# Kernel tuning notes

Hardware: AMD Instinct MI355X
Metric: run time of the kernel (lower is better)

Reference implementation:

```python
import jax, jax.numpy as jnp
import numpy as np

B, L, H, S, EXP = 8, 2048, 256, 64, 2
E = H * EXP

def setup_inputs() -> dict:
    key = jax.random.key(0)
    ks = jax.random.split(key, 12)
    u = jax.random.normal(ks[0], (B, L, H), dtype=jnp.float32)
    W_in = jax.random.normal(ks[1], (H, 2 * E), dtype=jnp.float32) * 0.02
    b_in = jax.random.normal(ks[2], (2 * E,), dtype=jnp.float32) * 0.02
    conv_w = jax.random.normal(ks[3], (E, 3), dtype=jnp.float32) * 0.3  # depthwise k=3
    conv_b = jax.random.normal(ks[4], (E,), dtype=jnp.float32) * 0.02
    W_x = jax.random.normal(ks[5], (E, 3 * S), dtype=jnp.float32) * 0.02
    b_x = jax.random.normal(ks[6], (3 * S,), dtype=jnp.float32) * 0.02
    A_log = jax.random.normal(ks[7], (S,), dtype=jnp.float32) * 0.1
    Dp = jnp.ones((E,), dtype=jnp.float32)
    W_out = jax.random.normal(ks[8], (E, H), dtype=jnp.float32) * 0.02
    b_out = jax.random.normal(ks[9], (H,), dtype=jnp.float32) * 0.02
    ln_g = jnp.ones((E,), dtype=jnp.float32)
    ln_b = jnp.zeros((E,), dtype=jnp.float32)
    return {"u": u, "W_in": W_in, "b_in": b_in, "conv_w": conv_w, "conv_b": conv_b,
            "W_x": W_x, "b_x": b_x, "A_log": A_log, "Dp": Dp,
            "W_out": W_out, "b_out": b_out, "ln_g": ln_g, "ln_b": ln_b}

def reference(u, W_in, b_in, conv_w, conv_b, W_x, b_x, A_log, Dp, W_out, b_out, ln_g, ln_b):
    Bb, Ll, Hh = u.shape
    Ss = A_log.shape[0]
    Ee = Dp.shape[0]
    xz = u @ W_in + b_in                      # [B,L,2E]
    x, z = jnp.split(xz, 2, axis=-1)          # [B,L,E] each
    # depthwise conv1d, kernel=3, padding=1 along L
    xp = jnp.pad(x, ((0, 0), (1, 1), (0, 0)))
    x = xp[:, :-2] * conv_w[:, 0] + xp[:, 1:-1] * conv_w[:, 1] + xp[:, 2:] * conv_w[:, 2] + conv_b
    x = jax.nn.silu(x)
    ssm = x @ W_x + b_x                       # [B,L,3S]
    delta, Bm, Cm = jnp.split(ssm, 3, axis=-1)
    delta = jax.nn.softplus(delta)            # [B,L,S]
    A = -jnp.exp(jnp.clip(A_log, -5.0, 5.0))  # [S]
    # torch broadcast quirk: delta[...,None] * A[None,None,:] -> [B,L,S,S], entry = delta[b,l,i]*A[j]
    A_d = jnp.exp(jnp.clip(delta[:, :, :, None] * A[None, None, None, :], -10.0, 0.0))  # [B,L,S,S]
    # bmm(B_discrete, x[:,t,:,None]) == (delta*B) * sum_e x, broadcast over E
    inp_term = (delta * Bm) * x.sum(-1, keepdims=True)  # [B,L,S]

    def step(h, inputs):
        A_t, it_t, C_t, x_t = inputs          # [B,S,S],[B,S],[B,S],[B,E]
        h = jnp.einsum('bij,bje->bie', A_t, h) + it_t[:, :, None]
        h = jnp.clip(h, -100.0, 100.0)
        y = jnp.einsum('bse,bs->be', h, C_t) + Dp * x_t
        return h, y

    h0 = jnp.zeros((Bb, Ss, Ee), dtype=u.dtype)
    xs = (jnp.swapaxes(A_d, 0, 1), jnp.swapaxes(inp_term, 0, 1),
          jnp.swapaxes(Cm, 0, 1), jnp.swapaxes(x, 0, 1))
    _, ys = jax.lax.scan(step, h0, xs)
    outputs = jnp.swapaxes(ys, 0, 1)          # [B,L,E]
    mu = outputs.mean(-1, keepdims=True)
    var = ((outputs - mu) ** 2).mean(-1, keepdims=True)
    y = (outputs - mu) / jnp.sqrt(var + 1e-5) * ln_g + ln_b
    y = y * jax.nn.silu(z)
    return y @ W_out + b_out  # dropout is identity in eval mode
```

## Files before the change

kernel.cpp:

```cpp
#include <hip/hip_runtime.h>
#include <hip/hip_bf16.h>

constexpr int BB = 8;
constexpr int LLEN = 2048;
constexpr int HH = 256;
constexpr int EE = 512;
constexpr int MM = BB * LLEN;

typedef short bf16x8 __attribute__((ext_vector_type(8)));
typedef float f32x4  __attribute__((ext_vector_type(4)));

static __device__ inline unsigned short f2bf(float f) {
    unsigned u = __builtin_bit_cast(unsigned, f);
    unsigned r = (u + 0x7FFFu + ((u >> 16) & 1u)) >> 16;
    return (unsigned short)r;
}
static __device__ inline float bf2f(unsigned short h) {
    return __builtin_bit_cast(float, (unsigned)h << 16);
}

#define GL2LDS(gp, lp) __builtin_amdgcn_global_load_lds( \
    (const __attribute__((address_space(1))) void*)(gp), \
    (__attribute__((address_space(3))) void*)(lp), 16, 0, 0)

__global__ __launch_bounds__(256) void cast_bf16_kernel(
    const float* __restrict__ in, unsigned short* __restrict__ out)
{
    int b = blockIdx.x;
    int cpx = gridDim.x >> 3;
    int lin = (b & 7) * cpx + (b >> 3);
    int i = (lin * 256 + threadIdx.x) * 4;
    float4 v = *reinterpret_cast<const float4*>(in + i);
    ushort4 o = {f2bf(v.x), f2bf(v.y), f2bf(v.z), f2bf(v.w)};
    *reinterpret_cast<ushort4*>(out + i) = o;
}

__global__ __launch_bounds__(256) void transpose_cast_kernel(
    const float* __restrict__ W, unsigned short* __restrict__ Wt, int K, int N)
{
    int i = blockIdx.x * 256 + threadIdx.x;
    if (i < K * N) {
        int n = i / K, k = i - n * K;
        Wt[i] = f2bf(W[(size_t)k * N + n]);
    }
}

__global__ __launch_bounds__(256) void k1_gemm(
    const unsigned short* __restrict__ A, const unsigned short* __restrict__ Bt,
    const float* __restrict__ bias,
    unsigned short* __restrict__ xb, unsigned short* __restrict__ zsb)
{
    __shared__ unsigned short Al[128 * 32];
    __shared__ unsigned short Bl[128 * 32];

    const int tid = threadIdx.x;
    const int lane = tid & 63;
    const int wave = tid >> 6;
    const int wrow = wave >> 1, wcol = wave & 1;
    const int l15 = lane & 15;
    const int lk  = lane >> 4;

    const int cpx = gridDim.x >> 3;
    int lin = blockIdx.x;
    lin = (lin & 7) * cpx + (lin >> 3);
    const int row0 = (lin >> 3) * 128;
    const int col0 = (lin & 7) * 128;
    const bool zside = col0 >= EE;
    unsigned short* Cp = zside ? zsb : xb;
    const int cb = zside ? col0 - EE : col0;

    f32x4 acc[4][4] = {};

    #pragma unroll
    for (int t = 0; t < 8; ++t) {
        const int kt = t * 32;
        #pragma unroll
        for (int i = 0; i < 2; ++i) {
            int sid = i * 256 + tid;
            int r = sid >> 2, o = sid & 3;
            GL2LDS(A + (size_t)(row0 + r) * 256 + kt + o * 8, &Al[sid * 8]);
        }
        #pragma unroll
        for (int i = 0; i < 2; ++i) {
            int sid = i * 256 + tid;
            int r = sid >> 2, o = sid & 3;
            GL2LDS(Bt + (size_t)(col0 + r) * 256 + kt + o * 8, &Bl[sid * 8]);
        }
        asm volatile("s_waitcnt vmcnt(0)" ::: "memory");
        __syncthreads();

        bf16x8 af[4], bfr[4];
        #pragma unroll
        for (int m = 0; m < 4; ++m) {
            const int r = wrow * 64 + m * 16 + l15;
            af[m] = *reinterpret_cast<const bf16x8*>(&Al[r * 32 + lk * 8]);
        }
        #pragma unroll
        for (int n = 0; n < 4; ++n) {
            const int r = wcol * 64 + n * 16 + l15;
            bfr[n] = *reinterpret_cast<const bf16x8*>(&Bl[r * 32 + lk * 8]);
        }
        #pragma unroll
        for (int m = 0; m < 4; ++m)
            #pragma unroll
            for (int n = 0; n < 4; ++n)
                acc[m][n] = __builtin_amdgcn_mfma_f32_16x16x32_bf16(
                    af[m], bfr[n], acc[m][n], 0, 0, 0);

        __syncthreads();
    }

    #pragma unroll
    for (int m = 0; m < 4; ++m) {
        #pragma unroll
        for (int n = 0; n < 4; ++n) {
            const int colloc = wcol * 64 + n * 16 + l15;
            const float bv = bias[col0 + colloc];
            #pragma unroll
            for (int i = 0; i < 4; ++i) {
                const int row = row0 + wrow * 64 + m * 16 + lk * 4 + i;
                float v = acc[m][n][i] + bv;
                if (zside) v = v / (1.f + __expf(-v));
                Cp[(size_t)row * EE + cb + colloc] = f2bf(v);
            }
        }
    }
}

__global__ __launch_bounds__(256, 1) void kb_mid_gemm3(
    const unsigned short* __restrict__ xb, const unsigned short* __restrict__ zsb,
    const unsigned short* __restrict__ Bt,
    const float* __restrict__ bias, float* __restrict__ out,
    const float* __restrict__ conv_w, const float* __restrict__ conv_b,
    const float* __restrict__ Dp, const float* __restrict__ ln_g,
    const float* __restrict__ ln_b)
{
    __shared__ unsigned short G[64 * 512];
    __shared__ unsigned short Bl[64 * 512];

    const int tid = threadIdx.x;
    const int lane = tid & 63;
    const int wave = tid >> 6;
    const int l15 = lane & 15;
    const int lk  = lane >> 4;

    const int b = blockIdx.x;
    const int lin = (b & 7) * 32 + (b >> 3);
    const int r0 = lin * 64;

    const int e0 = lane * 8;
    float cw0[8], cw1[8], cw2[8], cb8[8], dp8[8], lg8[8], lb8[8];
    #pragma unroll
    for (int j = 0; j < 8; ++j) {
        int e = e0 + j;
        cw0[j] = conv_w[e * 3 + 0];
        cw1[j] = conv_w[e * 3 + 1];
        cw2[j] = conv_w[e * 3 + 2];
        cb8[j] = conv_b[e];
        dp8[j] = Dp[e];
        lg8[j] = ln_g[e];
        lb8[j] = ln_b[e];
    }

    for (int it = 0; it < 16; ++it) {
        const int i = wave * 16 + it;
        const int gr = r0 + i;
        const int l = gr & (LLEN - 1);
        const size_t base = (size_t)gr * EE + e0;

        bf16x8 xc = *reinterpret_cast<const bf16x8*>(xb + base);
        bf16x8 xm = {}, xp = {};
        if (l > 0)        xm = *reinterpret_cast<const bf16x8*>(xb + base - EE);
        if (l < LLEN - 1) xp = *reinterpret_cast<const bf16x8*>(xb + base + EE);
        bf16x8 zv = *reinterpret_cast<const bf16x8*>(zsb + base);

        float o[8];
        float s1 = 0.f, s2 = 0.f;
        #pragma unroll
        for (int j = 0; j < 8; ++j) {
            float v = cb8[j]
                    + bf2f((unsigned short)xm[j]) * cw0[j]
                    + bf2f((unsigned short)xc[j]) * cw1[j]
                    + bf2f((unsigned short)xp[j]) * cw2[j];
            float sx = v / (1.f + __expf(-v));
            float oe = dp8[j] * sx;
            o[j] = oe;
            s1 += oe;
            s2 += oe * oe;
        }
        #pragma unroll
        for (int off = 1; off < 64; off <<= 1) {
            s1 += __shfl_xor(s1, off);
            s2 += __shfl_xor(s2, off);
        }
        const float mu  = s1 * (1.f / EE);
        const float var = s2 * (1.f / EE) - mu * mu;
        const float inv = rsqrtf(var + 1e-5f);

        bf16x8 gv;
        #pragma unroll
        for (int j = 0; j < 8; ++j) {
            float gy = ((o[j] - mu) * inv * lg8[j] + lb8[j]) * bf2f((unsigned short)zv[j]);
            gv[j] = (short)f2bf(gy);
        }
        *reinterpret_cast<bf16x8*>(&G[i * 512 + ((lane ^ (i & 7)) << 3)]) = gv;
    }

    bf16x8 breg[16];
    #pragma unroll
    for (int i = 0; i < 16; ++i) {
        int id = i * 256 + tid;
        breg[i] = *reinterpret_cast<const bf16x8*>(Bt + (size_t)id * 8);
    }
    __syncthreads();
    #pragma unroll
    for (int i = 0; i < 16; ++i) {
        int id = i * 256 + tid;
        int r = id >> 6, s = id & 63;
        *reinterpret_cast<bf16x8*>(&Bl[r * 512 + ((s ^ (r & 7)) << 3)]) = breg[i];
    }
    __syncthreads();

    const int wrow = wave >> 1, wcol = wave & 1;
    for (int c = 0; c < 4; ++c) {
        if (c < 3) {
            #pragma unroll
            for (int i = 0; i < 16; ++i) {
                int id = (c + 1) * 4096 + i * 256 + tid;
                breg[i] = *reinterpret_cast<const bf16x8*>(Bt + (size_t)id * 8);
            }
        }
        f32x4 acc[2][2] = {};
        #pragma unroll
        for (int ks = 0; ks < 16; ++ks) {
            bf16x8 af[2], bfr[2];
            #pragma unroll
            for (int m = 0; m < 2; ++m) {
                const int ra = wrow * 32 + m * 16 + l15;
                const int ph = (ks * 4 + lk) ^ (ra & 7);
                af[m] = *reinterpret_cast<const bf16x8*>(&G[ra * 512 + ph * 8]);
            }
            #pragma unroll
            for (int n = 0; n < 2; ++n) {
                const int rb = wcol * 32 + n * 16 + l15;
                const int ph = (ks * 4 + lk) ^ (rb & 7);
                bfr[n] = *reinterpret_cast<const bf16x8*>(&Bl[rb * 512 + ph * 8]);
            }
            #pragma unroll
            for (int m = 0; m < 2; ++m)
                #pragma unroll
                for (int n = 0; n < 2; ++n)
                    acc[m][n] = __builtin_amdgcn_mfma_f32_16x16x32_bf16(
                        af[m], bfr[n], acc[m][n], 0, 0, 0);
        }
        #pragma unroll
        for (int m = 0; m < 2; ++m) {
            #pragma unroll
            for (int n = 0; n < 2; ++n) {
                int col = c * 64 + wcol * 32 + n * 16 + l15;
                float bv = bias[col];
                #pragma unroll
                for (int i = 0; i < 4; ++i) {
                    int row = r0 + wrow * 32 + m * 16 + lk * 4 + i;
                    out[(size_t)row * HH + col] = acc[m][n][i] + bv;
                }
            }
        }
        if (c < 3) {
            __syncthreads();
            #pragma unroll
            for (int i = 0; i < 16; ++i) {
                int id = i * 256 + tid;
                int r = id >> 6, s = id & 63;
                *reinterpret_cast<bf16x8*>(&Bl[r * 512 + ((s ^ (r & 7)) << 3)]) = breg[i];
            }
            __syncthreads();
        }
    }
}

extern "C" void kernel_launch(void* const* d_in, const int* in_sizes, int n_in,
                              void* d_out, int out_size, void* d_ws, size_t ws_size,
                              hipStream_t stream)
{
    const float* u      = (const float*)d_in[0];
    const float* W_in   = (const float*)d_in[1];
    const float* b_in   = (const float*)d_in[2];
    const float* conv_w = (const float*)d_in[3];
    const float* conv_b = (const float*)d_in[4];
    const float* Dp     = (const float*)d_in[8];
    const float* W_out  = (const float*)d_in[9];
    const float* b_out  = (const float*)d_in[10];
    const float* ln_g   = (const float*)d_in[11];
    const float* ln_b   = (const float*)d_in[12];
    float* out = (float*)d_out;

    char* ws = (char*)d_ws;
    unsigned short* ubf   = (unsigned short*)ws; ws += (size_t)MM * HH * 2;
    unsigned short* wtin  = (unsigned short*)ws; ws += (size_t)1024 * HH * 2;
    unsigned short* wtout = (unsigned short*)ws; ws += (size_t)HH * EE * 2;
    unsigned short* xbuf  = (unsigned short*)ws; ws += (size_t)MM * EE * 2;
    unsigned short* zsbuf = (unsigned short*)ws;

    dim3 blk(256);

    transpose_cast_kernel<<<dim3((1024 * HH + 255) / 256), blk, 0, stream>>>(W_in, wtin, HH, 1024);
    transpose_cast_kernel<<<dim3((HH * EE + 255) / 256), blk, 0, stream>>>(W_out, wtout, EE, HH);
    cast_bf16_kernel<<<dim3(MM * HH / 1024), blk, 0, stream>>>(u, ubf);

    k1_gemm<<<dim3(1024), blk, 0, stream>>>(ubf, wtin, b_in, xbuf, zsbuf);

    kb_mid_gemm3<<<dim3(256), blk, 0, stream>>>(
        xbuf, zsbuf, wtout, b_out, out, conv_w, conv_b, Dp, ln_g, ln_b);
}
```

Measured before the change: 66.32 us.

## Fuse u bf16 cast into input GEMM with resident A row-block tiles

Removes the separate cast kernel and its bf16 copy of u. The input GEMM now loads a 64-row fp32 block of u, converts it to bf16 in-register and stores it in swizzled LDS once. It then loops over 8 column chunks of W_in with full K=256 held in LDS, using 512-thread blocks. This saves a global round trip of u, but the B-tile load is serialized with compute (no double buffering) and only 256 blocks are launched.

After: 67.35 us. About the same (+1.5%).

```diff
diff --git a/kernel.cpp b/kernel.cpp
--- a/kernel.cpp
+++ b/kernel.cpp
@@ -22,18 +22,6 @@
 #define GL2LDS(gp, lp) __builtin_amdgcn_global_load_lds( \
     (const __attribute__((address_space(1))) void*)(gp), \
     (__attribute__((address_space(3))) void*)(lp), 16, 0, 0)
-
-__global__ __launch_bounds__(256) void cast_bf16_kernel(
-    const float* __restrict__ in, unsigned short* __restrict__ out)
-{
-    int b = blockIdx.x;
-    int cpx = gridDim.x >> 3;
-    int lin = (b & 7) * cpx + (b >> 3);
-    int i = (lin * 256 + threadIdx.x) * 4;
-    float4 v = *reinterpret_cast<const float4*>(in + i);
-    ushort4 o = {f2bf(v.x), f2bf(v.y), f2bf(v.z), f2bf(v.w)};
-    *reinterpret_cast<ushort4*>(out + i) = o;
-}
 
 __global__ __launch_bounds__(256) void transpose_cast_kernel(
     const float* __restrict__ W, unsigned short* __restrict__ Wt, int K, int N)
@@ -45,85 +33,98 @@
     }
 }
 
-__global__ __launch_bounds__(256) void k1_gemm(
-    const unsigned short* __restrict__ A, const unsigned short* __restrict__ Bt,
+__global__ __launch_bounds__(512) void k1_kb(
+    const float* __restrict__ u, const unsigned short* __restrict__ Bt,
     const float* __restrict__ bias,
     unsigned short* __restrict__ xb, unsigned short* __restrict__ zsb)
 {
-    __shared__ unsigned short Al[128 * 32];
-    __shared__ unsigned short Bl[128 * 32];
+    __shared__ unsigned short Abuf[64 * 256];
+    __shared__ unsigned short Bbuf[128 * 256];
 
     const int tid = threadIdx.x;
     const int lane = tid & 63;
     const int wave = tid >> 6;
-    const int wrow = wave >> 1, wcol = wave & 1;
+    const int wrow = wave >> 2, wcol = wave & 3;
     const int l15 = lane & 15;
     const int lk  = lane >> 4;
 
-    const int cpx = gridDim.x >> 3;
-    int lin = blockIdx.x;
-    lin = (lin & 7) * cpx + (lin >> 3);
-    const int row0 = (lin >> 3) * 128;
-    const int col0 = (lin & 7) * 128;
-    const bool zside = col0 >= EE;
-    unsigned short* Cp = zside ? zsb : xb;
-    const int cb = zside ? col0 - EE : col0;
-
-    f32x4 acc[4][4] = {};
-
-    #pragma unroll
-    for (int t = 0; t < 8; ++t) {
-        const int kt = t * 32;
-        #pragma unroll
-        for (int i = 0; i < 2; ++i) {
-            int sid = i * 256 + tid;
-            int r = sid >> 2, o = sid & 3;
-            GL2LDS(A + (size_t)(row0 + r) * 256 + kt + o * 8, &Al[sid * 8]);
-        }
-        #pragma unroll
-        for (int i = 0; i < 2; ++i) {
-            int sid = i * 256 + tid;
-            int r = sid >> 2, o = sid & 3;
-            GL2LDS(Bt + (size_t)(col0 + r) * 256 + kt + o * 8, &Bl[sid * 8]);
+    const int b = blockIdx.x;
+    const int lin = (b & 7) * 32 + (b >> 3);
+    const int r0 = lin * 64;
+
+    #pragma unroll
+    for (int i = 0; i < 8; ++i) {
+        int sid = i * 512 + tid;
+        int cc = sid >> 5, s = sid & 31;
+        GL2LDS(Bt + (size_t)cc * 256 + ((s ^ (cc & 7)) << 3), &Bbuf[sid * 8]);
+    }
+    #pragma unroll
+    for (int i = 0; i < 8; ++i) {
+        int idx = i * 512 + tid;
+        int r = idx >> 6, c4 = idx & 63;
+        f32x4 v = *reinterpret_cast<const f32x4*>(u + (size_t)(r0 + r) * 256 + (c4 << 2));
+        ushort4 o = {f2bf(v[0]), f2bf(v[1]), f2bf(v[2]), f2bf(v[3])};
+        int off = r * 256 + ((((c4 >> 1) ^ (r & 7)) << 3) | ((c4 & 1) << 2));
+        *reinterpret_cast<ushort4*>(&Abuf[off]) = o;
+    }
+
+    for (int c = 0; c < 8; ++c) {
+        if (c > 0) {
+            #pragma unroll
+            for (int i = 0; i < 8; ++i) {
+                int sid = i * 512 + tid;
+                int cc = sid >> 5, s = sid & 31;
+                GL2LDS(Bt + (size_t)(c * 128 + cc) * 256 + ((s ^ (cc & 7)) << 3),
+                       &Bbuf[sid * 8]);
+            }
         }
         asm volatile("s_waitcnt vmcnt(0)" ::: "memory");
+        __builtin_amdgcn_sched_barrier(0);
         __syncthreads();
 
-        bf16x8 af[4], bfr[4];
-        #pragma unroll
-        for (int m = 0; m < 4; ++m) {
-            const int r = wrow * 64 + m * 16 + l15;
-            af[m] = *reinterpret_cast<const bf16x8*>(&Al[r * 32 + lk * 8]);
-        }
-        #pragma unroll
-        for (int n = 0; n < 4; ++n) {
-            const int r = wcol * 64 + n * 16 + l15;
-            bfr[n] = *reinterpret_cast<const bf16x8*>(&Bl[r * 32 + lk * 8]);
-        }
-        #pragma unroll
-        for (int m = 0; m < 4; ++m)
-            #pragma unroll
-            for (int n = 0; n < 4; ++n)
-                acc[m][n] = __builtin_amdgcn_mfma_f32_16x16x32_bf16(
-                    af[m], bfr[n], acc[m][n], 0, 0, 0);
-
+        f32x4 acc[2][2] = {};
+        #pragma unroll
+        for (int ks = 0; ks < 8; ++ks) {
+            bf16x8 af[2], bf[2];
+            #pragma unroll
+            for (int m = 0; m < 2; ++m) {
+                const int row = wrow * 32 + m * 16 + l15;
+                af[m] = *reinterpret_cast<const bf16x8*>(
+                    &Abuf[row * 256 + (((ks * 4 + lk) ^ (row & 7)) << 3)]);
+            }
+            #pragma unroll
+            for (int n = 0; n < 2; ++n) {
+                const int cl = wcol * 32 + n * 16 + l15;
+                bf[n] = *reinterpret_cast<const bf16x8*>(
+                    &Bbuf[cl * 256 + (((ks * 4 + lk) ^ (cl & 7)) << 3)]);
+            }
+            #pragma unroll
+            for (int m = 0; m < 2; ++m)
+                #pragma unroll
+                for (int n = 0; n < 2; ++n)
+                    acc[m][n] = __builtin_amdgcn_mfma_f32_16x16x32_bf16(
+                        af[m], bf[n], acc[m][n], 0, 0, 0);
+        }
+
+        const bool zside = c >= 4;
+        unsigned short* Cp = zside ? zsb : xb;
+        #pragma unroll
+        for (int m = 0; m < 2; ++m) {
+            #pragma unroll
+            for (int n = 0; n < 2; ++n) {
+                const int gcol = c * 128 + wcol * 32 + n * 16 + l15;
+                const float bv = bias[gcol];
+                const int ocol = gcol - (zside ? 512 : 0);
+                #pragma unroll
+                for (int i = 0; i < 4; ++i) {
+                    const int row = r0 + wrow * 32 + m * 16 + lk * 4 + i;
+                    float v = acc[m][n][i] + bv;
+                    if (zside) v = v / (1.f + __expf(-v));
+                    Cp[(size_t)row * EE + ocol] = f2bf(v);
+                }
+            }
+        }
         __syncthreads();
-    }
-
-    #pragma unroll
-    for (int m = 0; m < 4; ++m) {
-        #pragma unroll
-        for (int n = 0; n < 4; ++n) {
-            const int colloc = wcol * 64 + n * 16 + l15;
-            const float bv = bias[col0 + colloc];
-            #pragma unroll
-            for (int i = 0; i < 4; ++i) {
-                const int row = row0 + wrow * 64 + m * 16 + lk * 4 + i;
-                float v = acc[m][n][i] + bv;
-                if (zside) v = v / (1.f + __expf(-v));
-                Cp[(size_t)row * EE + cb + colloc] = f2bf(v);
-            }
-        }
     }
 }
 
@@ -296,7 +297,6 @@
     float* out = (float*)d_out;
 
     char* ws = (char*)d_ws;
-    unsigned short* ubf   = (unsigned short*)ws; ws += (size_t)MM * HH * 2;
     unsigned short* wtin  = (unsigned short*)ws; ws += (size_t)1024 * HH * 2;
     unsigned short* wtout = (unsigned short*)ws; ws += (size_t)HH * EE * 2;
     unsigned short* xbuf  = (unsigned short*)ws; ws += (size_t)MM * EE * 2;
@@ -306,9 +306,8 @@
 
     transpose_cast_kernel<<<dim3((1024 * HH + 255) / 256), blk, 0, stream>>>(W_in, wtin, HH, 1024);
     transpose_cast_kernel<<<dim3((HH * EE + 255) / 256), blk, 0, stream>>>(W_out, wtout, EE, HH);
-    cast_bf16_kernel<<<dim3(MM * HH / 1024), blk, 0, stream>>>(u, ubf);
-
-    k1_gemm<<<dim3(1024), blk, 0, stream>>>(ubf, wtin, b_in, xbuf, zsbuf);
+
+    k1_kb<<<dim3(256), dim3(512), 0, stream>>>(u, wtin, b_in, xbuf, zsbuf);
 
     kb_mid_gemm3<<<dim3(256), blk, 0, stream>>>(
         xbuf, zsbuf, wtout, b_out, out, conv_w, conv_b, Dp, ln_g, ln_b);
```
